# Kernel tuning notes

Hardware: AMD Instinct MI355X
Metric: run time of the kernel (lower is better)

The kernel has to match this reference:

```python
import jax, jax.numpy as jnp
import numpy as np

BATCH, IN, HID, NCLS = 4096, 2048, 8192, 1000

def setup_inputs() -> dict:
    key = jax.random.key(0)
    kx, kk, kg = jax.random.split(key, 3)
    x = jax.random.normal(kx, (BATCH, IN), dtype=jnp.float32)
    # torch nn.Linear weights: kohonen [HID, IN], grossberg [NCLS, HID], init U(-1, 1)
    Wk = jax.random.uniform(kk, (HID, IN), dtype=jnp.float32, minval=-1.0, maxval=1.0)
    Wg = jax.random.uniform(kg, (NCLS, HID), dtype=jnp.float32, minval=-1.0, maxval=1.0)
    return {"x": x, "Wk": Wk, "Wg": Wg}

def reference(x, Wk, Wg):
    # L2-normalize each row
    xn = x / jnp.linalg.norm(x, axis=1, keepdims=True)  # [B, IN]
    kohonen_out = jnp.einsum('bi,hi->bh', xn, Wk)        # [B, HID]
    idx = jnp.argmax(kohonen_out, axis=1)                # [B] winner units
    # one-hot @ Wg.T == gather columns of Wg for winning units
    out = jnp.take(Wg, idx, axis=1).T                    # [B, NCLS]
    return out
```

## Files before the change

kernel.cpp:

```cpp
#include <hip/hip_runtime.h>
#include <stdint.h>

typedef unsigned int u32;
typedef unsigned long long u64;
typedef unsigned short u16;
typedef unsigned char u8;
typedef int intx8 __attribute__((ext_vector_type(8)));
typedef float floatx4 __attribute__((ext_vector_type(4)));

#define BATCH 4096
#define IN    2048
#define HID   8192
#define NCLS  1000

#define OFF_ROWKEY 0u
#define OFF_TOPK   32768u
#define OFF_X8     8421376u
#define OFF_WK8    16809984u
#define OFF_WGT    33587200u
#define TOTAL_FULL 66355200ull

__device__ __forceinline__ u32 fkey(float f) {
    u32 u = __float_as_uint(f);
    return (u & 0x80000000u) ? ~u : (u | 0x80000000u);
}
__device__ __forceinline__ float unfkey(u32 k) {
    return __uint_as_float((k & 0x80000000u) ? (k ^ 0x80000000u) : ~k);
}
__device__ __forceinline__ void ce32(u32& a, u32& b) {
    u32 mx = a > b ? a : b;
    u32 mn = a > b ? b : a;
    a = mx; b = mn;
}

__global__ __launch_bounds__(256) void prep_kernel(
    const float* __restrict__ x, const float* __restrict__ Wk,
    const float* __restrict__ Wg,
    u8* __restrict__ x8, u8* __restrict__ wk8, float* __restrict__ WgT)
{
    __shared__ float t[32][33];
    const int bid = blockIdx.x;
    if (bid < 1024) {
        const int gid = bid * 256 + threadIdx.x;
        const int NSX = BATCH * IN / 16;
        const int NS  = NSX + HID * IN / 16;
        for (int s = gid; s < NS; s += 1024 * 256) {
            const float4* src; u8* dst;
            if (s < NSX) { src = (const float4*)x + (size_t)s * 4;  dst = x8  + (size_t)s * 16; }
            else { int u = s - NSX; src = (const float4*)Wk + (size_t)u * 4; dst = wk8 + (size_t)u * 16; }
            uint4 o;
            float4 f;
            int p;
            f = src[0];
            p = __builtin_amdgcn_cvt_pk_fp8_f32(f.x, f.y, 0, false);
            p = __builtin_amdgcn_cvt_pk_fp8_f32(f.z, f.w, p, true);  o.x = (u32)p;
            f = src[1];
            p = __builtin_amdgcn_cvt_pk_fp8_f32(f.x, f.y, 0, false);
            p = __builtin_amdgcn_cvt_pk_fp8_f32(f.z, f.w, p, true);  o.y = (u32)p;
            f = src[2];
            p = __builtin_amdgcn_cvt_pk_fp8_f32(f.x, f.y, 0, false);
            p = __builtin_amdgcn_cvt_pk_fp8_f32(f.z, f.w, p, true);  o.z = (u32)p;
            f = src[3];
            p = __builtin_amdgcn_cvt_pk_fp8_f32(f.x, f.y, 0, false);
            p = __builtin_amdgcn_cvt_pk_fp8_f32(f.z, f.w, p, true);  o.w = (u32)p;
            *(uint4*)dst = o;
        }
    } else {
        const int tb = bid - 1024;
        const int bx = (tb & 255) * 32;
        const int by = (tb >> 8) * 32;
        const int tx = threadIdx.x & 31, ty = threadIdx.x >> 5;
        #pragma unroll
        for (int i = 0; i < 32; i += 8) {
            int c = by + ty + i;
            t[ty + i][tx] = (c < NCLS) ? Wg[(size_t)c * HID + bx + tx] : 0.f;
        }
        __syncthreads();
        #pragma unroll
        for (int i = 0; i < 32; i += 8) {
            int c = by + tx;
            if (c < NCLS) WgT[(size_t)(bx + ty + i) * NCLS + by + tx] = t[tx][ty + i];
        }
    }
}

#define STG(gsrc, ldsoff) \
    __builtin_amdgcn_global_load_lds((const __attribute__((address_space(1))) u32*)(gsrc), \
        (__attribute__((address_space(3))) u32*)&LDS[ldsoff], 16, 0, 0)

#define MFMA1(A_, B_, C_) C_ = __builtin_amdgcn_mfma_scale_f32_16x16x128_f8f6f4( \
    A_, B_, C_, 0, 0, 0, 0x7F, 0, 0x7F)

__global__ __launch_bounds__(512, 2) void mfma_fp8_gemm_kernel(
    const u8* __restrict__ x8, const u8* __restrict__ wk8,
    u32* __restrict__ topk)
{
    __shared__ __align__(16) u8 LDS[2 * 65536];

    const int tid  = threadIdx.x;
    const int lane = tid & 63;
    const int w    = tid >> 6;
    const int bm   = blockIdx.y * 256;
    const int bn   = blockIdx.x * 256;
    const int wrow = (w >> 2) * 128;
    const int wcol = (w & 3) * 64;
    const int m = lane & 15, q = lane >> 4;

    floatx4 acc[8][4];
    #pragma unroll
    for (int i = 0; i < 8; i++)
        #pragma unroll
        for (int j = 0; j < 4; j++)
            acc[i][j] = (floatx4){0.f, 0.f, 0.f, 0.f};

    const int srow = tid >> 3;
    const int soff = (((((tid >> 1) & 3) ^ (srow & 3)) * 2) + (tid & 1)) * 16;
    const u8* gxa = x8  + (size_t)(bm + srow) * IN + soff;
    const u8* gwb = wk8 + (size_t)(bn + srow) * IN + soff;
    const u32 ldst = (u32)tid * 16;

    const u32 foq = (u32)((q ^ (m & 3)) * 32);

    STG(gxa,                      0u     + ldst);
    STG(gxa + 128 * (size_t)IN,   16384u + ldst);
    STG(gwb,                      32768u + ldst);
    STG(gwb +  64 * (size_t)IN,   40960u + ldst);
    STG(gwb + 128 * (size_t)IN,   49152u + ldst);
    STG(gwb + 192 * (size_t)IN,   57344u + ldst);
    STG(gxa +  64 * (size_t)IN,   8192u  + ldst);
    STG(gxa + 192 * (size_t)IN,   24576u + ldst);
    asm volatile("s_waitcnt vmcnt(2)" ::: "memory");
    __builtin_amdgcn_s_barrier();

    u32 cb = 0u;

    intx8 af[4], bf[4];

    #pragma unroll 1
    for (int kt = 0; kt < 16; ++kt) {
        const u32 nb = cb ^ 65536u;
        const size_t ko = (size_t)(kt + 1) * 128;
        #pragma unroll
        for (int i = 0; i < 4; i++)
            af[i] = *(const intx8*)&LDS[cb + (u32)(wrow + i * 16 + m) * 128u + foq];
        #pragma unroll
        for (int j = 0; j < 2; j++)
            bf[j] = *(const intx8*)&LDS[cb + 32768u + (u32)(wcol + j * 16 + m) * 128u + foq];
        if (kt < 15) {
            STG(gxa + ko,                     nb + ldst);
            STG(gxa + 128 * (size_t)IN + ko,  nb + 16384u + ldst);
        }
        asm volatile("" ::: "memory");
        __builtin_amdgcn_s_barrier();
        asm volatile("s_waitcnt lgkmcnt(0)" ::: "memory");
        __builtin_amdgcn_sched_barrier(0);
        __builtin_amdgcn_s_setprio(1);
        #pragma unroll
        for (int i = 0; i < 4; i++) { MFMA1(af[i], bf[0], acc[i][0]); }
        #pragma unroll
        for (int i = 0; i < 4; i++) { MFMA1(af[i], bf[1], acc[i][1]); }
        __builtin_amdgcn_s_setprio(0);
        asm volatile("" ::: "memory");
        __builtin_amdgcn_s_barrier();
        #pragma unroll
        for (int j = 2; j < 4; j++)
            bf[j] = *(const intx8*)&LDS[cb + 32768u + (u32)(wcol + j * 16 + m) * 128u + foq];
        if (kt < 15) {
            STG(gwb + ko,                     nb + 32768u + ldst);
            STG(gwb +  64 * (size_t)IN + ko,  nb + 40960u + ldst);
        }
        asm volatile("" ::: "memory");
        __builtin_amdgcn_s_barrier();
        asm volatile("s_waitcnt lgkmcnt(0)" ::: "memory");
        __builtin_amdgcn_sched_barrier(0);
        __builtin_amdgcn_s_setprio(1);
        #pragma unroll
        for (int i = 0; i < 4; i++) { MFMA1(af[i], bf[2], acc[i][2]); }
        #pragma unroll
        for (int i = 0; i < 4; i++) { MFMA1(af[i], bf[3], acc[i][3]); }
        __builtin_amdgcn_s_setprio(0);
        if (kt < 15) asm volatile("s_waitcnt vmcnt(4)" ::: "memory");
        else         asm volatile("s_waitcnt vmcnt(0)" ::: "memory");
        __builtin_amdgcn_s_barrier();
        #pragma unroll
        for (int i = 0; i < 4; i++)
            af[i] = *(const intx8*)&LDS[cb + (u32)(wrow + 64 + i * 16 + m) * 128u + foq];
        if (kt < 15) {
            STG(gwb + 128 * (size_t)IN + ko,  nb + 49152u + ldst);
            STG(gwb + 192 * (size_t)IN + ko,  nb + 57344u + ldst);
        }
        asm volatile("" ::: "memory");
        __builtin_amdgcn_s_barrier();
        asm volatile("s_waitcnt lgkmcnt(0)" ::: "memory");
        __builtin_amdgcn_sched_barrier(0);
        __builtin_amdgcn_s_setprio(1);
        #pragma unroll
        for (int i = 0; i < 4; i++) { MFMA1(af[i], bf[0], acc[4 + i][0]); }
        #pragma unroll
        for (int i = 0; i < 4; i++) { MFMA1(af[i], bf[1], acc[4 + i][1]); }
        __builtin_amdgcn_s_setprio(0);
        asm volatile("" ::: "memory");
        __builtin_amdgcn_s_barrier();
        if (kt < 15) {
            STG(gxa +  64 * (size_t)IN + ko,  nb + 8192u  + ldst);
            STG(gxa + 192 * (size_t)IN + ko,  nb + 24576u + ldst);
        }
        asm volatile("" ::: "memory");
        __builtin_amdgcn_s_barrier();
        __builtin_amdgcn_s_setprio(1);
        #pragma unroll
        for (int i = 0; i < 4; i++) { MFMA1(af[i], bf[2], acc[4 + i][2]); }
        #pragma unroll
        for (int i = 0; i < 4; i++) { MFMA1(af[i], bf[3], acc[4 + i][3]); }
        __builtin_amdgcn_s_setprio(0);
        if (kt < 15) asm volatile("s_waitcnt vmcnt(2)" ::: "memory");
        __builtin_amdgcn_s_barrier();
        cb = nb;
    }

    const int group = blockIdx.x * 4 + (w & 3);
    #pragma unroll
    for (int i = 0; i < 8; i++) {
        #pragma unroll
        for (int r = 0; r < 4; r++) {
            u32 k0 = (fkey(acc[i][0][r]) & 0xFFFFFFC0u) | (0u << 4) | (u32)m;
            u32 k1 = (fkey(acc[i][1][r]) & 0xFFFFFFC0u) | (1u << 4) | (u32)m;
            u32 k2 = (fkey(acc[i][2][r]) & 0xFFFFFFC0u) | (2u << 4) | (u32)m;
            u32 k3 = (fkey(acc[i][3][r]) & 0xFFFFFFC0u) | (3u << 4) | (u32)m;
            ce32(k0, k1); ce32(k2, k3); ce32(k0, k2); ce32(k1, k3); ce32(k1, k2);
            #pragma unroll
            for (int off = 1; off < 16; off <<= 1) {
                u32 b0 = __shfl_xor(k0, off, 64);
                u32 b1 = __shfl_xor(k1, off, 64);
                u32 b2 = __shfl_xor(k2, off, 64);
                u32 b3 = __shfl_xor(k3, off, 64);
                u32 t0 = k0 > b3 ? k0 : b3;
                u32 t1 = k1 > b2 ? k1 : b2;
                u32 t2 = k2 > b1 ? k2 : b1;
                u32 t3 = k3 > b0 ? k3 : b0;
                ce32(t0, t2); ce32(t1, t3); ce32(t0, t1); ce32(t2, t3);
                k0 = t0; k1 = t1; k2 = t2; k3 = t3;
            }
            if (m == 0) {
                const int grow = bm + wrow + i * 16 + q * 4 + r;
                uint4 v; v.x = k0; v.y = k1; v.z = k2; v.w = k3;
                *(uint4*)&topk[(size_t)grow * 512 + group * 4] = v;
            }
        }
    }
}

__global__ __launch_bounds__(256) void scan_kernel(
    const u32* __restrict__ topk,
    const float* __restrict__ x, const float* __restrict__ Wk,
    const float* __restrict__ WgT, float* __restrict__ out)
{
    __shared__ u16 cand[4][48];
    const int wv   = threadIdx.x >> 6;
    const int lane = threadIdx.x & 63;
    const int row  = blockIdx.x * 4 + wv;

    const uint4* tp = (const uint4*)(topk + (size_t)row * 512);
    uint4 v0 = tp[lane];
    uint4 v1 = tp[lane + 64];

    u32 mx = v0.x > v1.x ? v0.x : v1.x;
    #pragma unroll
    for (int off = 1; off < 64; off <<= 1) {
        u32 o = __shfl_xor(mx, off, 64);
        if (o > mx) mx = o;
    }
    const float thr = unfkey(mx & 0xFFFFFFC0u) - 12.0f;

    int base = 0;
    const u32 ks[8] = {v0.x, v0.y, v0.z, v0.w, v1.x, v1.y, v1.z, v1.w};
    #pragma unroll
    for (int s = 0; s < 8; s++) {
        const int group = (s < 4) ? lane : (lane + 64);
        const u32 key = ks[s];
        const bool in = unfkey(key & 0xFFFFFFC0u) >= thr;
        const u64 msk = __ballot(in);
        if (in) {
            int rnk = base + __popcll(msk & ((1ull << lane) - 1ull));
            if (rnk < 48)
                cand[wv][rnk] = (u16)(group * 64 + (int)((key >> 4) & 3u) * 16 + (int)(key & 15u));
        }
        base += __popcll(msk);
    }
    const int n = min(base, 48);
    __builtin_amdgcn_wave_barrier();

    int col;
    if (n <= 1) {
        col = cand[wv][0];
    } else {
        const float4* xr = (const float4*)(x + (size_t)row * IN);
        float4 a[8];
        #pragma unroll
        for (int p = 0; p < 8; p++) a[p] = xr[p * 64 + lane];
        u64 best = 0ull;
        for (int c = 0; c < n; c++) {
            const int h = cand[wv][c];
            const float4* wr = (const float4*)(Wk + (size_t)h * IN);
            float s = 0.f;
            #pragma unroll
            for (int p = 0; p < 8; p++) {
                float4 b = wr[p * 64 + lane];
                s += a[p].x * b.x + a[p].y * b.y + a[p].z * b.z + a[p].w * b.w;
            }
            #pragma unroll
            for (int off = 1; off < 64; off <<= 1) s += __shfl_xor(s, off, 64);
            u64 key = ((u64)fkey(s) << 32) | (u64)(0x1FFFu - (u32)h);
            if (key > best) best = key;
        }
        col = 0x1FFF - (int)(best & 0xFFFFu);
    }

    const float4* src = (const float4*)(WgT + (size_t)col * NCLS);
    float4* dst = (float4*)(out + (size_t)row * NCLS);
    for (int t = lane; t < NCLS / 4; t += 64) dst[t] = src[t];
}

__global__ void init_ws_kernel(u64* rowkey) {
    int i = blockIdx.x * blockDim.x + threadIdx.x;
    if (i < BATCH) rowkey[i] = 0ULL;
}

__global__ __launch_bounds__(256) void gemm_argmax_kernel(
    const float* __restrict__ x, const float* __restrict__ Wk,
    u64* __restrict__ rowkey)
{
    __shared__ __align__(16) float As[32 * 64];
    __shared__ __align__(16) float Bs[32 * 64];
    const int tid = threadIdx.x;
    const int bm = blockIdx.y * 64, bn = blockIdx.x * 64;
    const int tx = tid & 15, ty = tid >> 4;
    float acc[4][4];
    #pragma unroll
    for (int i = 0; i < 4; i++)
        #pragma unroll
        for (int j = 0; j < 4; j++) acc[i][j] = 0.f;
    const int r0 = tid >> 3, q0 = tid & 7;
    const int r1 = (tid + 256) >> 3, q1 = (tid + 256) & 7;
    const float* xA0 = &x[(size_t)(bm + r0) * IN + q0 * 4];
    const float* xA1 = &x[(size_t)(bm + r1) * IN + q1 * 4];
    const float* wB0 = &Wk[(size_t)(bn + r0) * IN + q0 * 4];
    const float* wB1 = &Wk[(size_t)(bn + r1) * IN + q1 * 4];
    for (int k0 = 0; k0 < IN; k0 += 32) {
        float4 a0 = *(const float4*)(xA0 + k0);
        float4 a1 = *(const float4*)(xA1 + k0);
        float4 b0 = *(const float4*)(wB0 + k0);
        float4 b1 = *(const float4*)(wB1 + k0);
        __syncthreads();
        As[(q0 * 4 + 0) * 64 + r0] = a0.x; As[(q0 * 4 + 1) * 64 + r0] = a0.y;
        As[(q0 * 4 + 2) * 64 + r0] = a0.z; As[(q0 * 4 + 3) * 64 + r0] = a0.w;
        As[(q1 * 4 + 0) * 64 + r1] = a1.x; As[(q1 * 4 + 1) * 64 + r1] = a1.y;
        As[(q1 * 4 + 2) * 64 + r1] = a1.z; As[(q1 * 4 + 3) * 64 + r1] = a1.w;
        Bs[(q0 * 4 + 0) * 64 + r0] = b0.x; Bs[(q0 * 4 + 1) * 64 + r0] = b0.y;
        Bs[(q0 * 4 + 2) * 64 + r0] = b0.z; Bs[(q0 * 4 + 3) * 64 + r0] = b0.w;
        Bs[(q1 * 4 + 0) * 64 + r1] = b1.x; Bs[(q1 * 4 + 1) * 64 + r1] = b1.y;
        Bs[(q1 * 4 + 2) * 64 + r1] = b1.z; Bs[(q1 * 4 + 3) * 64 + r1] = b1.w;
        __syncthreads();
        #pragma unroll
        for (int k = 0; k < 32; k++) {
            float4 av = *(const float4*)&As[k * 64 + ty * 4];
            float4 bv = *(const float4*)&Bs[k * 64 + tx * 4];
            acc[0][0] += av.x * bv.x; acc[0][1] += av.x * bv.y;
            acc[0][2] += av.x * bv.z; acc[0][3] += av.x * bv.w;
            acc[1][0] += av.y * bv.x; acc[1][1] += av.y * bv.y;
            acc[1][2] += av.y * bv.z; acc[1][3] += av.y * bv.w;
            acc[2][0] += av.z * bv.x; acc[2][1] += av.z * bv.y;
            acc[2][2] += av.z * bv.z; acc[2][3] += av.z * bv.w;
            acc[3][0] += av.w * bv.x; acc[3][1] += av.w * bv.y;
            acc[3][2] += av.w * bv.z; acc[3][3] += av.w * bv.w;
        }
    }
    #pragma unroll
    for (int i = 0; i < 4; i++) {
        const int row = bm + ty * 4 + i;
        u64 best = 0ULL;
        #pragma unroll
        for (int j = 0; j < 4; j++) {
            const int col = bn + tx * 4 + j;
            u64 p = ((u64)fkey(acc[i][j]) << 32) | (u64)(0x1FFFu - (unsigned)col);
            if (p > best) best = p;
        }
        #pragma unroll
        for (int off = 1; off < 16; off <<= 1) {
            u64 other = __shfl_xor(best, off, 64);
            if (other > best) best = other;
        }
        if (tx == 0) atomicMax(&rowkey[row], best);
    }
}

__global__ __launch_bounds__(256) void gather_kernel(
    const u64* __restrict__ rowkey, const float* __restrict__ Wg,
    float* __restrict__ out)
{
    const int b = blockIdx.y;
    const int c = blockIdx.x * 256 + threadIdx.x;
    if (c >= NCLS) return;
    const int col = 0x1FFF - (int)(rowkey[b] & 0xFFFFFFFFu);
    out[(size_t)b * NCLS + c] = Wg[(size_t)c * HID + col];
}

extern "C" void kernel_launch(void* const* d_in, const int* in_sizes, int n_in,
                              void* d_out, int out_size, void* d_ws, size_t ws_size,
                              hipStream_t stream) {
    const float* x  = (const float*)d_in[0];
    const float* Wk = (const float*)d_in[1];
    const float* Wg = (const float*)d_in[2];
    float* out = (float*)d_out;
    char* ws = (char*)d_ws;

    if (ws_size >= TOTAL_FULL) {
        u32* topk  = (u32*)(ws + OFF_TOPK);
        u8*  x8    = (u8*)(ws + OFF_X8);
        u8*  wk8   = (u8*)(ws + OFF_WK8);
        float* WgT = (float*)(ws + OFF_WGT);

        hipLaunchKernelGGL(prep_kernel, dim3(1024 + 8192), dim3(256), 0, stream,
                           x, Wk, Wg, x8, wk8, WgT);
        hipLaunchKernelGGL(mfma_fp8_gemm_kernel, dim3(HID / 256, BATCH / 256), dim3(512), 0, stream,
                           x8, wk8, topk);
        hipLaunchKernelGGL(scan_kernel, dim3(BATCH / 4), dim3(256), 0, stream,
                           topk, x, Wk, WgT, out);
    } else {
        u64* rowkey = (u64*)(ws + OFF_ROWKEY);
        hipLaunchKernelGGL(init_ws_kernel, dim3(16), dim3(256), 0, stream, rowkey);
        hipLaunchKernelGGL(gemm_argmax_kernel, dim3(HID / 64, BATCH / 64), dim3(256), 0, stream,
                           x, Wk, rowkey);
        hipLaunchKernelGGL(gather_kernel, dim3(4, BATCH), dim3(256), 0, stream,
                           rowkey, Wg, out);
    }
}
```

Before: 318.1 us.

## Simplify FP8 GEMM main loop to one barrier per K-step with XOR-8 swizzle

The LDS swizzle changes from a 4-way 32-byte XOR to an 8-way 16-byte XOR, and each fragment is now read as two 16-byte LDS loads, to cut bank conflicts. The interleaved four-phase schedule, which had many barriers and staggered global-to-LDS stages, becomes one phase that issues all eight prefetches up front, runs two MFMA blocks, then waits on vmcnt(0) and a single barrier. Fewer barriers and simpler scheduling are traded for less fine-grained overlap of loads with compute and a full drain of the memory queue every iteration.

```diff
diff --git a/kernel.cpp b/kernel.cpp
--- a/kernel.cpp
+++ b/kernel.cpp
@@ -5,6 +5,7 @@
 typedef unsigned long long u64;
 typedef unsigned short u16;
 typedef unsigned char u8;
+typedef int intx4 __attribute__((ext_vector_type(4)));
 typedef int intx8 __attribute__((ext_vector_type(8)));
 typedef float floatx4 __attribute__((ext_vector_type(4)));
 
@@ -88,6 +89,11 @@
     __builtin_amdgcn_global_load_lds((const __attribute__((address_space(1))) u32*)(gsrc), \
         (__attribute__((address_space(3))) u32*)&LDS[ldsoff], 16, 0, 0)
 
+#define RD8(dst, off) { \
+    intx4 lo_ = *(const intx4*)&LDS[(off)]; \
+    intx4 hi_ = *(const intx4*)&LDS[(off) ^ 16u]; \
+    dst = __builtin_shufflevector(lo_, hi_, 0, 1, 2, 3, 4, 5, 6, 7); }
+
 #define MFMA1(A_, B_, C_) C_ = __builtin_amdgcn_mfma_scale_f32_16x16x128_f8f6f4( \
     A_, B_, C_, 0, 0, 0, 0x7F, 0, 0x7F)
 
@@ -114,107 +120,76 @@
             acc[i][j] = (floatx4){0.f, 0.f, 0.f, 0.f};
 
     const int srow = tid >> 3;
-    const int soff = (((((tid >> 1) & 3) ^ (srow & 3)) * 2) + (tid & 1)) * 16;
+    const int soff = ((tid & 7) ^ (srow & 7)) * 16;
     const u8* gxa = x8  + (size_t)(bm + srow) * IN + soff;
     const u8* gwb = wk8 + (size_t)(bn + srow) * IN + soff;
     const u32 ldst = (u32)tid * 16;
 
-    const u32 foq = (u32)((q ^ (m & 3)) * 32);
+    const u32 csel = (u32)((((2 * q) ^ (m & 7))) * 16);
+    const u32 rdA  = (u32)(wrow + m) * 128u + csel;
+    const u32 rdB  = 32768u + (u32)(wcol + m) * 128u + csel;
 
     STG(gxa,                      0u     + ldst);
+    STG(gxa +  64 * (size_t)IN,   8192u  + ldst);
     STG(gxa + 128 * (size_t)IN,   16384u + ldst);
+    STG(gxa + 192 * (size_t)IN,   24576u + ldst);
     STG(gwb,                      32768u + ldst);
     STG(gwb +  64 * (size_t)IN,   40960u + ldst);
     STG(gwb + 128 * (size_t)IN,   49152u + ldst);
     STG(gwb + 192 * (size_t)IN,   57344u + ldst);
-    STG(gxa +  64 * (size_t)IN,   8192u  + ldst);
-    STG(gxa + 192 * (size_t)IN,   24576u + ldst);
-    asm volatile("s_waitcnt vmcnt(2)" ::: "memory");
+    asm volatile("s_waitcnt vmcnt(0)" ::: "memory");
     __builtin_amdgcn_s_barrier();
 
     u32 cb = 0u;
-
     intx8 af[4], bf[4];
 
     #pragma unroll 1
     for (int kt = 0; kt < 16; ++kt) {
         const u32 nb = cb ^ 65536u;
         const size_t ko = (size_t)(kt + 1) * 128;
-        #pragma unroll
-        for (int i = 0; i < 4; i++)
-            af[i] = *(const intx8*)&LDS[cb + (u32)(wrow + i * 16 + m) * 128u + foq];
-        #pragma unroll
-        for (int j = 0; j < 2; j++)
-            bf[j] = *(const intx8*)&LDS[cb + 32768u + (u32)(wcol + j * 16 + m) * 128u + foq];
+        RD8(af[0], cb + rdA);
+        RD8(af[1], cb + rdA + 2048u);
+        RD8(af[2], cb + rdA + 4096u);
+        RD8(af[3], cb + rdA + 6144u);
+        RD8(bf[0], cb + rdB);
+        RD8(bf[1], cb + rdB + 2048u);
+        RD8(bf[2], cb + rdB + 4096u);
+        RD8(bf[3], cb + rdB + 6144u);
         if (kt < 15) {
-            STG(gxa + ko,                     nb + ldst);
+            STG(gxa + ko,                     nb          + ldst);
+            STG(gxa +  64 * (size_t)IN + ko,  nb + 8192u  + ldst);
             STG(gxa + 128 * (size_t)IN + ko,  nb + 16384u + ldst);
-        }
-        asm volatile("" ::: "memory");
-        __builtin_amdgcn_s_barrier();
+            STG(gxa + 192 * (size_t)IN + ko,  nb + 24576u + ldst);
+            STG(gwb + ko,                     nb + 32768u + ldst);
+            STG(gwb +  64 * (size_t)IN + ko,  nb + 40960u + ldst);
+            STG(gwb + 128 * (size_t)IN + ko,  nb + 49152u + ldst);
+            STG(gwb + 192 * (size_t)IN + ko,  nb + 57344u + ldst);
+        }
         asm volatile("s_waitcnt lgkmcnt(0)" ::: "memory");
         __builtin_amdgcn_sched_barrier(0);
         __builtin_amdgcn_s_setprio(1);
         #pragma unroll
-        for (int i = 0; i < 4; i++) { MFMA1(af[i], bf[0], acc[i][0]); }
-        #pragma unroll
-        for (int i = 0; i < 4; i++) { MFMA1(af[i], bf[1], acc[i][1]); }
+        for (int j = 0; j < 4; j++)
+            #pragma unroll
+            for (int i = 0; i < 4; i++) { MFMA1(af[i], bf[j], acc[i][j]); }
         __builtin_amdgcn_s_setprio(0);
-        asm volatile("" ::: "memory");
-        __builtin_amdgcn_s_barrier();
-        #pragma unroll
-        for (int j = 2; j < 4; j++)
-            bf[j] = *(const intx8*)&LDS[cb + 32768u + (u32)(wcol + j * 16 + m) * 128u + foq];
-        if (kt < 15) {
-            STG(gwb + ko,                     nb + 32768u + ldst);
-            STG(gwb +  64 * (size_t)IN + ko,  nb + 40960u + ldst);
-        }
-        asm volatile("" ::: "memory");
-        __builtin_amdgcn_s_barrier();
+        __builtin_amdgcn_sched_barrier(0);
+        RD8(af[0], cb + rdA + 8192u);
+        RD8(af[1], cb + rdA + 10240u);
+        RD8(af[2], cb + rdA + 12288u);
+        RD8(af[3], cb + rdA + 14336u);
         asm volatile("s_waitcnt lgkmcnt(0)" ::: "memory");
         __builtin_amdgcn_sched_barrier(0);
         __builtin_amdgcn_s_setprio(1);
         #pragma unroll
-        for (int i = 0; i < 4; i++) { MFMA1(af[i], bf[2], acc[i][2]); }
-        #pragma unroll
-        for (int i = 0; i < 4; i++) { MFMA1(af[i], bf[3], acc[i][3]); }
+        for (int j = 0; j < 4; j++)
+            #pragma unroll
+            for (int i = 0; i < 4; i++) { MFMA1(af[i], bf[j], acc[4 + i][j]); }
         __builtin_amdgcn_s_setprio(0);
-        if (kt < 15) asm volatile("s_waitcnt vmcnt(4)" ::: "memory");
-        else         asm volatile("s_waitcnt vmcnt(0)" ::: "memory");
-        __builtin_amdgcn_s_barrier();
-        #pragma unroll
-        for (int i = 0; i < 4; i++)
-            af[i] = *(const intx8*)&LDS[cb + (u32)(wrow + 64 + i * 16 + m) * 128u + foq];
         if (kt < 15) {
-            STG(gwb + 128 * (size_t)IN + ko,  nb + 49152u + ldst);
-            STG(gwb + 192 * (size_t)IN + ko,  nb + 57344u + ldst);
-        }
-        asm volatile("" ::: "memory");
-        __builtin_amdgcn_s_barrier();
-        asm volatile("s_waitcnt lgkmcnt(0)" ::: "memory");
-        __builtin_amdgcn_sched_barrier(0);
-        __builtin_amdgcn_s_setprio(1);
-        #pragma unroll
-        for (int i = 0; i < 4; i++) { MFMA1(af[i], bf[0], acc[4 + i][0]); }
-        #pragma unroll
-        for (int i = 0; i < 4; i++) { MFMA1(af[i], bf[1], acc[4 + i][1]); }
-        __builtin_amdgcn_s_setprio(0);
-        asm volatile("" ::: "memory");
-        __builtin_amdgcn_s_barrier();
-        if (kt < 15) {
-            STG(gxa +  64 * (size_t)IN + ko,  nb + 8192u  + ldst);
-            STG(gxa + 192 * (size_t)IN + ko,  nb + 24576u + ldst);
-        }
-        asm volatile("" ::: "memory");
-        __builtin_amdgcn_s_barrier();
-        __builtin_amdgcn_s_setprio(1);
-        #pragma unroll
-        for (int i = 0; i < 4; i++) { MFMA1(af[i], bf[2], acc[4 + i][2]); }
-        #pragma unroll
-        for (int i = 0; i < 4; i++) { MFMA1(af[i], bf[3], acc[4 + i][3]); }
-        __builtin_amdgcn_s_setprio(0);
-        if (kt < 15) asm volatile("s_waitcnt vmcnt(2)" ::: "memory");
-        __builtin_amdgcn_s_barrier();
+            asm volatile("s_waitcnt vmcnt(0)" ::: "memory");
+            __builtin_amdgcn_s_barrier();
+        }
         cb = nb;
     }
 
```

After: 306.6 us. -3.6%, faster.
